# Optimization experiments

Hardware: AMD Instinct MI355X
Metric: run time of the kernel (lower is better)

## Reference

```python
import jax, jax.numpy as jnp
import numpy as np

SEQ_LEN = 8192
INPUT_SIZE = 2048
HIDDEN_SIZE = 2048


def _xavier(key, out_f, in_f):
    # xavier_uniform_ bound = sqrt(6 / (fan_in + fan_out))
    bound = np.sqrt(6.0 / (in_f + out_f)).astype(np.float32)
    return jax.random.uniform(key, (out_f, in_f), jnp.float32, -bound, bound)


def setup_inputs() -> dict:
    key = jax.random.key(0)
    k_x, k_wi, k_bi, k_wh, k_bh = jax.random.split(key, 5)
    x = jax.random.normal(k_x, (SEQ_LEN, INPUT_SIZE), jnp.float32)
    Wi = _xavier(k_wi, HIDDEN_SIZE, INPUT_SIZE)
    bi = jax.random.uniform(k_bi, (HIDDEN_SIZE,), jnp.float32)
    Wh = _xavier(k_wh, HIDDEN_SIZE, HIDDEN_SIZE)
    bh = jax.random.uniform(k_bh, (HIDDEN_SIZE,), jnp.float32)
    return {"x": x, "Wi": Wi, "bi": bi, "Wh": Wh, "bh": bh}


def reference(x, Wi, bi, Wh, bh):
    # Precompute the input projection for all timesteps as one GEMM: [S, H]
    x_proj = x @ Wi.T + bi

    def step(h, xt):
        # h_t = tanh(i2h(x_t) + h2h(h_{t-1}))
        h_new = jnp.tanh(xt + h @ Wh.T + bh)
        return h_new, h_new

    h0 = jnp.zeros((Wh.shape[0],), dtype=x.dtype)
    h_n, outputs = jax.lax.scan(step, h0, x_proj)
    # outputs: [S, H] hidden states; h_n: [H] final hidden state
    return outputs, h_n
```

## Files before the change

kernel.cpp:

```cpp
#include <hip/hip_runtime.h>
#include <hip/hip_bf16.h>

#define SEQ 8192
#define HID 2048
#define NBLK 64
#define ROWS 32

typedef short short8 __attribute__((ext_vector_type(8)));
typedef float floatx4 __attribute__((ext_vector_type(4)));

__device__ __forceinline__ void split_bf16(const float* __restrict__ p,
                                           short8& hi, short8& lo) {
    const float4 f0 = *(const float4*)p;
    const float4 f1 = *(const float4*)(p + 4);
    const float f[8] = {f0.x, f0.y, f0.z, f0.w, f1.x, f1.y, f1.z, f1.w};
#pragma unroll
    for (int e = 0; e < 8; ++e) {
        const unsigned u = __float_as_uint(f[e]);
        const unsigned r = (u + 0x7fffu + ((u >> 16) & 1u)) & 0xffff0000u;
        hi[e] = (short)(r >> 16);
        const float l = f[e] - __uint_as_float(r);
        const unsigned ul = __float_as_uint(l);
        lo[e] = (short)((ul + 0x7fffu + ((ul >> 16) & 1u)) >> 16);
    }
}

__global__ __launch_bounds__(256) void xproj_gemm(
    const float* __restrict__ x,
    const float* __restrict__ Wi,
    const float* __restrict__ bi,
    float* __restrict__ xp)
{
    const int bn = blockIdx.x;
    const int bm = blockIdx.y;
    const int tid = threadIdx.x;
    const int wave = tid >> 6;
    const int lane = tid & 63;
    const int wM = wave & 1, wN = wave >> 1;
    const int l16 = lane & 15, kq = lane >> 4;
    const int m0 = bm * 64 + wM * 32;
    const int n0 = bn * 64 + wN * 32;

    floatx4 acc00 = {0.f,0.f,0.f,0.f}, acc01 = {0.f,0.f,0.f,0.f};
    floatx4 acc10 = {0.f,0.f,0.f,0.f}, acc11 = {0.f,0.f,0.f,0.f};

    const float* xA0 = x  + (size_t)(m0 + l16)      * HID;
    const float* xA1 = x  + (size_t)(m0 + 16 + l16) * HID;
    const float* wB0 = Wi + (size_t)(n0 + l16)      * HID;
    const float* wB1 = Wi + (size_t)(n0 + 16 + l16) * HID;

    for (int kc = 0; kc < HID; kc += 32) {
        const int k = kc + kq * 8;
        short8 a0h, a0l, a1h, a1l, b0h, b0l, b1h, b1l;
        split_bf16(xA0 + k, a0h, a0l);
        split_bf16(xA1 + k, a1h, a1l);
        split_bf16(wB0 + k, b0h, b0l);
        split_bf16(wB1 + k, b1h, b1l);
        acc00 = __builtin_amdgcn_mfma_f32_16x16x32_bf16(a0h, b0h, acc00, 0,0,0);
        acc00 = __builtin_amdgcn_mfma_f32_16x16x32_bf16(a0l, b0h, acc00, 0,0,0);
        acc00 = __builtin_amdgcn_mfma_f32_16x16x32_bf16(a0h, b0l, acc00, 0,0,0);
        acc01 = __builtin_amdgcn_mfma_f32_16x16x32_bf16(a0h, b1h, acc01, 0,0,0);
        acc01 = __builtin_amdgcn_mfma_f32_16x16x32_bf16(a0l, b1h, acc01, 0,0,0);
        acc01 = __builtin_amdgcn_mfma_f32_16x16x32_bf16(a0h, b1l, acc01, 0,0,0);
        acc10 = __builtin_amdgcn_mfma_f32_16x16x32_bf16(a1h, b0h, acc10, 0,0,0);
        acc10 = __builtin_amdgcn_mfma_f32_16x16x32_bf16(a1l, b0h, acc10, 0,0,0);
        acc10 = __builtin_amdgcn_mfma_f32_16x16x32_bf16(a1h, b0l, acc10, 0,0,0);
        acc11 = __builtin_amdgcn_mfma_f32_16x16x32_bf16(a1h, b1h, acc11, 0,0,0);
        acc11 = __builtin_amdgcn_mfma_f32_16x16x32_bf16(a1l, b1h, acc11, 0,0,0);
        acc11 = __builtin_amdgcn_mfma_f32_16x16x32_bf16(a1h, b1l, acc11, 0,0,0);
    }

    const float bi0 = bi[n0 + l16];
    const float bi1 = bi[n0 + 16 + l16];
#pragma unroll
    for (int reg = 0; reg < 4; ++reg) {
        const int mlo = m0 + kq * 4 + reg;
        const int mhi = mlo + 16;
        xp[(size_t)mlo * HID + n0 + l16]      = acc00[reg] + bi0;
        xp[(size_t)mlo * HID + n0 + 16 + l16] = acc01[reg] + bi1;
        xp[(size_t)mhi * HID + n0 + l16]      = acc10[reg] + bi0;
        xp[(size_t)mhi * HID + n0 + 16 + l16] = acc11[reg] + bi1;
    }
}

__global__ __launch_bounds__(512, 1) void rnn_scan(
    const float* __restrict__ Wh,
    const float* __restrict__ bh,
    const float* __restrict__ xp,
    unsigned long long* hbuf,
    float* out)
{
    __shared__ float h_lds[HID];

    const int b   = blockIdx.x;
    const int tid = threadIdx.x;
    const int wv  = tid >> 6;
    const int L   = tid & 63;

    float w[4][8][4];
#pragma unroll
    for (int r = 0; r < 4; ++r) {
        const size_t row = (size_t)(b * ROWS + wv * 4 + r);
#pragma unroll
        for (int j = 0; j < 8; ++j) {
            const float4 pk = *(const float4*)(Wh + row * HID + 256 * j + 4 * L);
            w[r][j][0] = pk.x; w[r][j][1] = pk.y;
            w[r][j][2] = pk.z; w[r][j][3] = pk.w;
        }
    }
    const float bh_l = (L < 4) ? bh[b * ROWS + wv * 4 + L] : 0.f;

    for (int t = 0; t < SEQ; ++t) {
        float xp_l = 0.f;
        if (L < 4) xp_l = xp[(size_t)t * HID + b * ROWS + wv * 4 + L];

        float acc[4] = {0.f, 0.f, 0.f, 0.f};

        if (t > 0) {
            const unsigned long long* src = hbuf + ((t - 1) & 1) * HID;
            const int want = t - 1;
#pragma unroll
            for (int q = 0; q < 4; ++q) {
                const int idx = 4 * tid + q;
                unsigned long long v;
                do {
                    v = __hip_atomic_load(src + idx, __ATOMIC_RELAXED,
                                          __HIP_MEMORY_SCOPE_AGENT);
                } while ((int)(v >> 32) != want);
                h_lds[idx] = __uint_as_float((unsigned)v);
            }
            __syncthreads();
#pragma unroll
            for (int j = 0; j < 8; ++j) {
                const float4 hv = *(const float4*)&h_lds[256 * j + 4 * L];
#pragma unroll
                for (int r = 0; r < 4; ++r) {
                    acc[r] += w[r][j][0] * hv.x;
                    acc[r] += w[r][j][1] * hv.y;
                    acc[r] += w[r][j][2] * hv.z;
                    acc[r] += w[r][j][3] * hv.w;
                }
            }
        }

#pragma unroll
        for (int off = 32; off > 0; off >>= 1) {
#pragma unroll
            for (int r = 0; r < 4; ++r) acc[r] += __shfl_xor(acc[r], off, 64);
        }

        if (L < 4) {
            const int row = b * ROWS + wv * 4 + L;
            float a = acc[L] + xp_l + bh_l;
            a = fminf(fmaxf(a, -15.f), 15.f);
            const float e = __expf(2.f * a);
            const float hval = (e - 1.f) / (e + 1.f);
            const unsigned long long tagged =
                ((unsigned long long)(unsigned)t << 32) |
                (unsigned long long)__float_as_uint(hval);
            __hip_atomic_store(&hbuf[(t & 1) * HID + row], tagged,
                               __ATOMIC_RELAXED, __HIP_MEMORY_SCOPE_AGENT);
            out[(size_t)t * HID + row] = hval;
            if (t == SEQ - 1)
                out[(size_t)SEQ * HID + row] = hval;
        }
    }
}

extern "C" void kernel_launch(void* const* d_in, const int* in_sizes, int n_in,
                              void* d_out, int out_size, void* d_ws, size_t ws_size,
                              hipStream_t stream) {
    const float* x  = (const float*)d_in[0];
    const float* Wi = (const float*)d_in[1];
    const float* bi = (const float*)d_in[2];
    const float* Wh = (const float*)d_in[3];
    const float* bh = (const float*)d_in[4];
    float* out      = (float*)d_out;

    float* xp = (float*)d_ws;
    unsigned long long* hbuf = (unsigned long long*)(xp + (size_t)SEQ * HID);

    xproj_gemm<<<dim3(HID / 64, SEQ / 64), 256, 0, stream>>>(x, Wi, bi, xp);
    rnn_scan<<<NBLK, 512, 0, stream>>>(Wh, bh, xp, hbuf, out);
}
```

Baseline: 23.68 ms.

## Vectorize tagged hidden-state polling and defer output stores off critical path

```diff
diff --git a/kernel.cpp b/kernel.cpp
--- a/kernel.cpp
+++ b/kernel.cpp
@@ -8,6 +8,7 @@
 
 typedef short short8 __attribute__((ext_vector_type(8)));
 typedef float floatx4 __attribute__((ext_vector_type(4)));
+typedef unsigned uintx4 __attribute__((ext_vector_type(4)));
 
 __device__ __forceinline__ void split_bf16(const float* __restrict__ p,
                                            short8& hi, short8& lo) {
@@ -96,40 +97,52 @@
     const int tid = threadIdx.x;
     const int wv  = tid >> 6;
     const int L   = tid & 63;
-
-    float w[4][8][4];
+    const int row = b * ROWS + wv * 4 + L;
+
+    floatx4 w[4][8];
 #pragma unroll
     for (int r = 0; r < 4; ++r) {
-        const size_t row = (size_t)(b * ROWS + wv * 4 + r);
-#pragma unroll
-        for (int j = 0; j < 8; ++j) {
-            const float4 pk = *(const float4*)(Wh + row * HID + 256 * j + 4 * L);
-            w[r][j][0] = pk.x; w[r][j][1] = pk.y;
-            w[r][j][2] = pk.z; w[r][j][3] = pk.w;
-        }
-    }
-    const float bh_l = (L < 4) ? bh[b * ROWS + wv * 4 + L] : 0.f;
+        const size_t rr = (size_t)(b * ROWS + wv * 4 + r);
+#pragma unroll
+        for (int j = 0; j < 8; ++j)
+            w[r][j] = *(const floatx4*)(Wh + rr * HID + 256 * j + 4 * L);
+    }
+    const float bh_l = (L < 4) ? bh[row] : 0.f;
+
+    float xp_cur = (L < 4) ? xp[row] : 0.f;
+    float prev_h = 0.f;
 
     for (int t = 0; t < SEQ; ++t) {
-        float xp_l = 0.f;
-        if (L < 4) xp_l = xp[(size_t)t * HID + b * ROWS + wv * 4 + L];
-
         float acc[4] = {0.f, 0.f, 0.f, 0.f};
 
         if (t > 0) {
             const unsigned long long* src = hbuf + ((t - 1) & 1) * HID;
-            const int want = t - 1;
-#pragma unroll
-            for (int q = 0; q < 4; ++q) {
-                const int idx = 4 * tid + q;
-                unsigned long long v;
-                do {
-                    v = __hip_atomic_load(src + idx, __ATOMIC_RELAXED,
-                                          __HIP_MEMORY_SCOPE_AGENT);
-                } while ((int)(v >> 32) != want);
-                h_lds[idx] = __uint_as_float((unsigned)v);
-            }
-            __syncthreads();
+            const unsigned want = (unsigned)(t - 1);
+            const unsigned long long* s0 = src + 2 * tid;
+            const unsigned long long* s1 = src + 1024 + 2 * tid;
+            uintx4 p0, p1;
+            do {
+                asm volatile(
+                    "global_load_dwordx4 %0, %2, off sc0 sc1\n\t"
+                    "global_load_dwordx4 %1, %3, off sc0 sc1\n\t"
+                    "s_waitcnt vmcnt(0)"
+                    : "=&v"(p0), "=&v"(p1)
+                    : "v"(s0), "v"(s1)
+                    : "memory");
+            } while ((p0[1] != want) | (p0[3] != want) |
+                     (p1[1] != want) | (p1[3] != want));
+            *(float2*)&h_lds[2 * tid] =
+                make_float2(__uint_as_float(p0[0]), __uint_as_float(p0[2]));
+            *(float2*)&h_lds[1024 + 2 * tid] =
+                make_float2(__uint_as_float(p1[0]), __uint_as_float(p1[2]));
+            if (L < 4) out[(size_t)(t - 1) * HID + row] = prev_h;
+            asm volatile("s_waitcnt lgkmcnt(0)\n\ts_barrier" ::: "memory");
+        }
+
+        float xp_next = 0.f;
+        if (L < 4 && t + 1 < SEQ) xp_next = xp[(size_t)(t + 1) * HID + row];
+
+        if (t > 0) {
 #pragma unroll
             for (int j = 0; j < 8; ++j) {
                 const float4 hv = *(const float4*)&h_lds[256 * j + 4 * L];
@@ -150,8 +163,7 @@
         }
 
         if (L < 4) {
-            const int row = b * ROWS + wv * 4 + L;
-            float a = acc[L] + xp_l + bh_l;
+            float a = acc[L] + xp_cur + bh_l;
             a = fminf(fmaxf(a, -15.f), 15.f);
             const float e = __expf(2.f * a);
             const float hval = (e - 1.f) / (e + 1.f);
@@ -160,10 +172,14 @@
                 (unsigned long long)__float_as_uint(hval);
             __hip_atomic_store(&hbuf[(t & 1) * HID + row], tagged,
                                __ATOMIC_RELAXED, __HIP_MEMORY_SCOPE_AGENT);
-            out[(size_t)t * HID + row] = hval;
-            if (t == SEQ - 1)
-                out[(size_t)SEQ * HID + row] = hval;
-        }
+            prev_h = hval;
+        }
+        xp_cur = xp_next;
+    }
+
+    if (L < 4) {
+        out[(size_t)(SEQ - 1) * HID + row] = prev_h;
+        out[(size_t)SEQ * HID + row]       = prev_h;
     }
 }
 
```

Result: faster. 20.61 ms (-13.0%).
